# Optimization experiments

Measured on AMD Instinct MI355X. Metric: run time of the kernel, lower is better.

The kernel has to match this reference:

```python
import jax, jax.numpy as jnp
import numpy as np

N_EMBD = 384
N_HEAD = 6
HEAD_DIM = N_EMBD // N_HEAD


def setup_inputs() -> dict:
    key = jax.random.key(0)
    k1, k2, k3, k4, k5 = jax.random.split(key, 5)
    B, T, C = 256, 165, N_EMBD
    x = jax.random.normal(k1, (B, T, C), dtype=jnp.float32)
    # nn.Linear stores weight as [out, in]; we keep [in, out] for x @ W
    s = 1.0 / np.sqrt(C)
    w_qkv = jax.random.uniform(k2, (C, 3 * C), minval=-s, maxval=s, dtype=jnp.float32)
    b_qkv = jax.random.uniform(k3, (3 * C,), minval=-s, maxval=s, dtype=jnp.float32)
    w_proj = jax.random.uniform(k4, (C, C), minval=-s, maxval=s, dtype=jnp.float32)
    b_proj = jax.random.uniform(k5, (C,), minval=-s, maxval=s, dtype=jnp.float32)
    return {"x": x, "w_qkv": w_qkv, "b_qkv": b_qkv, "w_proj": w_proj, "b_proj": b_proj}


def _attn(x, w_qkv, b_qkv, w_proj, b_proj):
    B, T, C = x.shape
    qkv = x @ w_qkv + b_qkv                      # [B, T, 3C]
    q, k, v = jnp.split(qkv, 3, axis=-1)
    def heads(t):
        return t.reshape(B, T, N_HEAD, HEAD_DIM).transpose(0, 2, 1, 3)  # [B,H,T,D]
    q, k, v = heads(q), heads(k), heads(v)
    scale = 1.0 / np.sqrt(HEAD_DIM)
    scores = jnp.einsum("bhqd,bhkd->bhqk", q, k) * scale  # [B,H,T,T]
    # mask: all True except last row attends only to the last column
    row = jnp.arange(T)[:, None]
    col = jnp.arange(T)[None, :]
    allowed = (row != T - 1) | (col == T - 1)              # [T,T] bool
    scores = jnp.where(allowed, scores, -jnp.inf)
    attn = jax.nn.softmax(scores, axis=-1)
    y = jnp.einsum("bhqk,bhkd->bhqd", attn, v)             # [B,H,T,D]
    y = y.transpose(0, 2, 1, 3).reshape(B, T, C)
    return y @ w_proj + b_proj


def reference(x, w_qkv, b_qkv, w_proj, b_proj):
    return _attn(x, w_qkv, b_qkv, w_proj, b_proj)
```

## Files before the change

### kernel.cpp

```cpp
#include <hip/hip_runtime.h>


typedef __attribute__((ext_vector_type(8))) short s16x8;
typedef __attribute__((ext_vector_type(4))) float f32x4;

__device__ __forceinline__ ushort f2b(float f) {
  union { float f; unsigned u; } v; v.f = f;
  unsigned u = v.u;
  return (ushort)((u + 0x7FFFu + ((u >> 16) & 1u)) >> 16);
}

__device__ __forceinline__ void gload_lds16(const ushort* g, ushort* l) {
  __builtin_amdgcn_global_load_lds((const __attribute__((address_space(1))) void*)g,
                                   (__attribute__((address_space(3))) void*)l, 16, 0, 0);
}

__global__ __launch_bounds__(256) void prep(const float* __restrict__ x,
                                            const float* __restrict__ wq,
                                            const float* __restrict__ wp,
                                            ushort* __restrict__ xb,
                                            ushort* __restrict__ wqT,
                                            ushort* __restrict__ wpT)
{
  const int stride = gridDim.x * 256;
  const int i0 = blockIdx.x * 256 + threadIdx.x;
  for (int i = i0; i < 4055040; i += stride) {
    float4 v = ((const float4*)x)[i];
    ushort4 h = make_ushort4(f2b(v.x), f2b(v.y), f2b(v.z), f2b(v.w));
    ((ushort4*)xb)[i] = h;
  }
  for (int i = i0; i < 110592; i += stride) {
    const int n = i / 96, k4 = (i % 96) * 4;
    ushort4 h = make_ushort4(f2b(wq[(size_t)(k4 + 0) * 1152 + n]),
                             f2b(wq[(size_t)(k4 + 1) * 1152 + n]),
                             f2b(wq[(size_t)(k4 + 2) * 1152 + n]),
                             f2b(wq[(size_t)(k4 + 3) * 1152 + n]));
    *(ushort4*)(wqT + (size_t)n * 384 + k4) = h;
  }
  for (int i = i0; i < 36864; i += stride) {
    const int n = i / 96, k4 = (i % 96) * 4;
    ushort4 h = make_ushort4(f2b(wp[(size_t)(k4 + 0) * 384 + n]),
                             f2b(wp[(size_t)(k4 + 1) * 384 + n]),
                             f2b(wp[(size_t)(k4 + 2) * 384 + n]),
                             f2b(wp[(size_t)(k4 + 3) * 384 + n]));
    *(ushort4*)(wpT + (size_t)n * 384 + k4) = h;
  }
}

template<int NB, int NOUT, bool OUT_F32>
__global__ __launch_bounds__(256) void gemm_bias(const ushort* __restrict__ A,
                                                 const ushort* __restrict__ Bt,
                                                 const float* __restrict__ bias,
                                                 void* __restrict__ Out)
{
  __shared__ __align__(16) ushort Asm[2][128][64];
  __shared__ __align__(16) ushort Bsm[2][128][64];
  const int tid  = threadIdx.x;
  const int lane = tid & 63;
  const int wave = tid >> 6;
  const int wr = wave >> 1, wc = wave & 1;

  const int nwg = gridDim.x;
  const int qch = nwg >> 3, rch = nwg & 7;
  const int xcd = blockIdx.x & 7, idx = blockIdx.x >> 3;
  const int nl = (xcd < rch) ? xcd * (qch + 1) + idx
                             : rch * (qch + 1) + (xcd - rch) * qch + idx;
  const int n0 = (nl % NB) * 128;
  const int m0 = (nl / NB) * 128;

  const ushort* Ag = A  + (size_t)(m0 + (tid >> 3)) * 384 + ((tid & 7) << 3);
  const ushort* Bg = Bt + (size_t)(n0 + (tid >> 3)) * 384 + ((tid & 7) << 3);

  f32x4 acc[4][4] = {};

#define STAGE(buf, k0)                                              \
  {                                                                 \
    ushort* at_ = (ushort*)Asm[buf] + tid * 8;                      \
    ushort* bt_ = (ushort*)Bsm[buf] + tid * 8;                      \
    _Pragma("unroll")                                               \
    for (int i = 0; i < 4; ++i) {                                   \
      gload_lds16(Ag + (k0) + i * 32 * 384, at_ + i * 2048);        \
      gload_lds16(Bg + (k0) + i * 32 * 384, bt_ + i * 2048);        \
    }                                                               \
  }

  STAGE(0, 0);
  #pragma unroll
  for (int t = 0; t < 6; ++t) {
    const int cur = t & 1;
    if (t < 5) {
      STAGE(cur ^ 1, (t + 1) * 64);
      asm volatile("s_waitcnt vmcnt(8)" ::: "memory");
    } else {
      asm volatile("s_waitcnt vmcnt(0)" ::: "memory");
    }
    __builtin_amdgcn_s_barrier();
    #pragma unroll
    for (int ks = 0; ks < 2; ++ks) {
      const int kk = (ks << 5) + ((lane >> 4) << 3);
      s16x8 a[4], b[4];
      #pragma unroll
      for (int mi = 0; mi < 4; ++mi)
        a[mi] = *(const s16x8*)(&Asm[cur][(wr << 6) + (mi << 4) + (lane & 15)][kk]);
      #pragma unroll
      for (int ni = 0; ni < 4; ++ni)
        b[ni] = *(const s16x8*)(&Bsm[cur][(wc << 6) + (ni << 4) + (lane & 15)][kk]);
      #pragma unroll
      for (int mi = 0; mi < 4; ++mi) {
        #pragma unroll
        for (int ni = 0; ni < 4; ++ni)
          acc[mi][ni] = __builtin_amdgcn_mfma_f32_16x16x32_bf16(a[mi], b[ni], acc[mi][ni], 0, 0, 0);
      }
    }
    __builtin_amdgcn_s_barrier();
  }
#undef STAGE

  #pragma unroll
  for (int mi = 0; mi < 4; ++mi) {
    #pragma unroll
    for (int ni = 0; ni < 4; ++ni) {
      const int col = n0 + (wc << 6) + (ni << 4) + (lane & 15);
      const float bv = bias[col];
      #pragma unroll
      for (int r = 0; r < 4; ++r) {
        const int row = m0 + (wr << 6) + (mi << 4) + ((lane >> 4) << 2) + r;
        const float v = acc[mi][ni][r] + bv;
        if (OUT_F32) ((float*)Out)[(size_t)row * NOUT + col] = v;
        else         ((ushort*)Out)[(size_t)row * NOUT + col] = f2b(v);
      }
    }
  }
}

__global__ __launch_bounds__(256) void attn_kernel(const ushort* __restrict__ QKV,
                                                   ushort* __restrict__ Y)
{
  __shared__ __align__(16) ushort Ksm[165][64];
  __shared__ __align__(16) ushort Vtsm[64][168];
  __shared__ __align__(16) ushort Psm[4][16][168];
  const int bh = blockIdx.x;
  const int b = bh / 6, h = bh % 6;
  const int tid = threadIdx.x, lane = tid & 63, wave = tid >> 6;
  const size_t base = (size_t)b * 165 * 1152 + (size_t)h * 64;

  for (int idx = tid; idx < 165 * 8; idx += 256) {
    const int t = idx >> 3, d8 = (idx & 7) << 3;
    *(uint4*)(&Ksm[t][d8]) = *(const uint4*)(QKV + base + (size_t)t * 1152 + 384 + d8);
  }
  for (int idx = tid; idx < 165 * 8; idx += 256) {
    const int t = idx >> 3, d8 = (idx & 7) << 3;
    uint4 v = *(const uint4*)(QKV + base + (size_t)t * 1152 + 768 + d8);
    const ushort* pv = (const ushort*)&v;
    #pragma unroll
    for (int j = 0; j < 8; ++j) Vtsm[d8 + j][t] = pv[j];
  }
  for (int idx = tid; idx < 64 * 3; idx += 256) Vtsm[idx / 3][165 + idx % 3] = 0;
  __syncthreads();

  const int colv = lane & 15;
  const int grp  = lane >> 4;
  for (int it = 0; it < 3; ++it) {
    const int qt = wave + (it << 2);
    const bool active = qt < 11;
    if (active) {
      const int tq = qt * 16 + colv;
      const int tqc = tq > 164 ? 164 : tq;
      const ushort* qrow = QKV + base + (size_t)tqc * 1152;
      const s16x8 qf0 = *(const s16x8*)(qrow + (grp << 3));
      const s16x8 qf1 = *(const s16x8*)(qrow + 32 + (grp << 3));
      f32x4 s[11];
      #pragma unroll
      for (int ct = 0; ct < 11; ++ct) {
        const int col = ct * 16 + colv;
        s16x8 kb0 = {}, kb1 = {};
        if (col < 165) {
          kb0 = *(const s16x8*)(&Ksm[col][grp << 3]);
          kb1 = *(const s16x8*)(&Ksm[col][32 + (grp << 3)]);
        }
        f32x4 a = {};
        a = __builtin_amdgcn_mfma_f32_16x16x32_bf16(qf0, kb0, a, 0, 0, 0);
        a = __builtin_amdgcn_mfma_f32_16x16x32_bf16(qf1, kb1, a, 0, 0, 0);
        s[ct] = a * 0.125f;
      }
      #pragma unroll
      for (int r = 0; r < 4; ++r) {
        float m = -1e30f;
        #pragma unroll
        for (int ct = 0; ct < 11; ++ct)
          if (ct * 16 + colv < 165) m = fmaxf(m, s[ct][r]);
        #pragma unroll
        for (int off = 1; off < 16; off <<= 1) m = fmaxf(m, __shfl_xor(m, off));
        float sum = 0.f;
        #pragma unroll
        for (int ct = 0; ct < 11; ++ct) {
          const float p = (ct * 16 + colv < 165) ? __expf(s[ct][r] - m) : 0.f;
          s[ct][r] = p;
          sum += p;
        }
        #pragma unroll
        for (int off = 1; off < 16; off <<= 1) sum += __shfl_xor(sum, off);
        const float inv = 1.f / sum;
        #pragma unroll
        for (int ct = 0; ct < 11; ++ct) s[ct][r] *= inv;
      }
      #pragma unroll
      for (int ct = 0; ct < 11; ++ct) {
        const int col = ct * 16 + colv;
        if (col < 168) {
          #pragma unroll
          for (int r = 0; r < 4; ++r)
            Psm[wave][(grp << 2) + r][col] = f2b(s[ct][r]);
        }
      }
    }
    __syncthreads();
    if (active) {
      f32x4 ya[4] = {};
      #pragma unroll
      for (int ksv = 0; ksv < 6; ++ksv) {
        const int kk = (ksv << 5) + (grp << 3);
        s16x8 pa = {};
        if (kk <= 160) pa = *(const s16x8*)(&Psm[wave][colv][kk]);
        #pragma unroll
        for (int nt = 0; nt < 4; ++nt) {
          s16x8 vb = {};
          if (kk <= 160) vb = *(const s16x8*)(&Vtsm[nt * 16 + colv][kk]);
          ya[nt] = __builtin_amdgcn_mfma_f32_16x16x32_bf16(pa, vb, ya[nt], 0, 0, 0);
        }
      }
      #pragma unroll
      for (int nt = 0; nt < 4; ++nt) {
        #pragma unroll
        for (int r = 0; r < 4; ++r) {
          const int trow = qt * 16 + (grp << 2) + r;
          if (trow < 165) {
            const int d = nt * 16 + colv;
            ushort val;
            if (trow == 164) val = QKV[base + (size_t)164 * 1152 + 768 + d];
            else             val = f2b(ya[nt][r]);
            Y[((size_t)b * 165 + trow) * 384 + h * 64 + d] = val;
          }
        }
      }
    }
    __syncthreads();
  }
}

extern "C" void kernel_launch(void* const* d_in, const int* in_sizes, int n_in,
                              void* d_out, int out_size, void* d_ws, size_t ws_size,
                              hipStream_t stream) {
  const float* x      = (const float*)d_in[0];
  const float* w_qkv  = (const float*)d_in[1];
  const float* b_qkv  = (const float*)d_in[2];
  const float* w_proj = (const float*)d_in[3];
  const float* b_proj = (const float*)d_in[4];
  float* out = (float*)d_out;

  char* ws = (char*)d_ws;
  ushort* xb  = (ushort*)ws;
  ushort* wqT = (ushort*)(ws + 32440320);
  ushort* wpT = (ushort*)(ws + 33325056);
  ushort* qkv = (ushort*)(ws + 33619968);
  ushort* y   = xb;

  prep<<<1024, 256, 0, stream>>>(x, w_qkv, w_proj, xb, wqT, wpT);
  gemm_bias<9, 1152, false><<<2970, 256, 0, stream>>>(xb, wqT, b_qkv, qkv);
  attn_kernel<<<1536, 256, 0, stream>>>(qkv, y);
  gemm_bias<3, 384, true><<<990, 256, 0, stream>>>(y, wpT, b_proj, out);
}
```

Before: 261.2 us.

## Compute transposed scores in registers and feed P directly to PV MFMA

The attention kernel now computes S^T (K as the A operand) so each lane holds a full key column slice, which lets P be packed to bf16 in registers and fed straight into 16x16x16 MFMAs without the Psm shared-memory round trip or the mid-loop barriers. K is read directly from global instead of being staged in LDS, and V is staged as paired-bf16 32-bit words. Softmax uses exp2 with a folded log2e scale, rcp, and packed bf16 conversion instructions, and occupancy is hinted with launch_bounds(256,4). The risk is that uncached global K reads repeat across waves, and the smaller MFMA shape issues more instructions.

```diff
diff --git a/kernel.cpp b/kernel.cpp
--- a/kernel.cpp
+++ b/kernel.cpp
@@ -2,6 +2,7 @@
 
 
 typedef __attribute__((ext_vector_type(8))) short s16x8;
+typedef __attribute__((ext_vector_type(4))) short s16x4;
 typedef __attribute__((ext_vector_type(4))) float f32x4;
 
 __device__ __forceinline__ ushort f2b(float f) {
@@ -14,6 +15,29 @@
   __builtin_amdgcn_global_load_lds((const __attribute__((address_space(1))) void*)g,
                                    (__attribute__((address_space(3))) void*)l, 16, 0, 0);
 }
+
+#if __has_builtin(__builtin_amdgcn_mfma_f32_16x16x16bf16_1k)
+__device__ __forceinline__ f32x4 mfma16x16x16(s16x4 a, s16x4 b, f32x4 c) {
+  return __builtin_amdgcn_mfma_f32_16x16x16bf16_1k(a, b, c, 0, 0, 0);
+}
+#else
+__device__ __forceinline__ f32x4 mfma16x16x16(s16x4 a, s16x4 b, f32x4 c) {
+  asm("v_mfma_f32_16x16x16_bf16 %0, %1, %2, %0" : "+v"(c) : "v"(a), "v"(b));
+  return c;
+}
+#endif
+
+#if __has_builtin(__builtin_amdgcn_exp2f)
+#define EXP2F(x) __builtin_amdgcn_exp2f(x)
+#else
+#define EXP2F(x) __expf((x) * 0.6931471805599453f)
+#endif
+
+#if __has_builtin(__builtin_amdgcn_rcpf)
+#define RCPF(x) __builtin_amdgcn_rcpf(x)
+#else
+#define RCPF(x) (1.0f / (x))
+#endif
 
 __global__ __launch_bounds__(256) void prep(const float* __restrict__ x,
                                             const float* __restrict__ wq,
@@ -133,118 +157,125 @@
   }
 }
 
-__global__ __launch_bounds__(256) void attn_kernel(const ushort* __restrict__ QKV,
-                                                   ushort* __restrict__ Y)
+__global__ __launch_bounds__(256, 4) void attn_kernel(const ushort* __restrict__ QKV,
+                                                      ushort* __restrict__ Y)
 {
-  __shared__ __align__(16) ushort Ksm[165][64];
-  __shared__ __align__(16) ushort Vtsm[64][168];
-  __shared__ __align__(16) ushort Psm[4][16][168];
+  __shared__ uint Vt32[64][85];
   const int bh = blockIdx.x;
   const int b = bh / 6, h = bh % 6;
   const int tid = threadIdx.x, lane = tid & 63, wave = tid >> 6;
+  const int colv = lane & 15, grp = lane >> 4;
   const size_t base = (size_t)b * 165 * 1152 + (size_t)h * 64;
-
-  for (int idx = tid; idx < 165 * 8; idx += 256) {
-    const int t = idx >> 3, d8 = (idx & 7) << 3;
-    *(uint4*)(&Ksm[t][d8]) = *(const uint4*)(QKV + base + (size_t)t * 1152 + 384 + d8);
-  }
-  for (int idx = tid; idx < 165 * 8; idx += 256) {
-    const int t = idx >> 3, d8 = (idx & 7) << 3;
-    uint4 v = *(const uint4*)(QKV + base + (size_t)t * 1152 + 768 + d8);
-    const ushort* pv = (const ushort*)&v;
-    #pragma unroll
-    for (int j = 0; j < 8; ++j) Vtsm[d8 + j][t] = pv[j];
-  }
-  for (int idx = tid; idx < 64 * 3; idx += 256) Vtsm[idx / 3][165 + idx % 3] = 0;
+  const ushort* Vg = QKV + base + 768;
+
+  for (int idx = tid; idx < 85 * 8; idx += 256) {
+    const int tp = idx >> 3, d8 = (idx & 7) << 3;
+    const int t0 = 2 * tp, t1 = t0 + 1;
+    uint4 a  = *(const uint4*)(Vg + (size_t)(t0 > 164 ? 164 : t0) * 1152 + d8);
+    uint4 bv = *(const uint4*)(Vg + (size_t)(t1 > 164 ? 164 : t1) * 1152 + d8);
+    if (t0 > 164) a  = make_uint4(0, 0, 0, 0);
+    if (t1 > 164) bv = make_uint4(0, 0, 0, 0);
+    const ushort* au = (const ushort*)&a;
+    const ushort* bu = (const ushort*)&bv;
+    #pragma unroll
+    for (int j = 0; j < 8; ++j)
+      Vt32[d8 + j][tp] = (uint)au[j] | ((uint)bu[j] << 16);
+  }
   __syncthreads();
 
-  const int colv = lane & 15;
-  const int grp  = lane >> 4;
   for (int it = 0; it < 3; ++it) {
     const int qt = wave + (it << 2);
-    const bool active = qt < 11;
-    if (active) {
-      const int tq = qt * 16 + colv;
-      const int tqc = tq > 164 ? 164 : tq;
-      const ushort* qrow = QKV + base + (size_t)tqc * 1152;
-      const s16x8 qf0 = *(const s16x8*)(qrow + (grp << 3));
-      const s16x8 qf1 = *(const s16x8*)(qrow + 32 + (grp << 3));
-      f32x4 s[11];
-      #pragma unroll
-      for (int ct = 0; ct < 11; ++ct) {
-        const int col = ct * 16 + colv;
-        s16x8 kb0 = {}, kb1 = {};
-        if (col < 165) {
-          kb0 = *(const s16x8*)(&Ksm[col][grp << 3]);
-          kb1 = *(const s16x8*)(&Ksm[col][32 + (grp << 3)]);
+    if (qt >= 11) continue;
+    const int qrow = qt * 16 + colv;
+    const ushort* qp = QKV + base + (size_t)(qrow > 164 ? 164 : qrow) * 1152;
+    const s16x8 qf0 = *(const s16x8*)(qp + (grp << 3));
+    const s16x8 qf1 = *(const s16x8*)(qp + 32 + (grp << 3));
+
+    f32x4 s[11];
+    #pragma unroll
+    for (int ct = 0; ct < 11; ++ct) {
+      const int kr = ct * 16 + colv;
+      const ushort* kp = QKV + base + (size_t)(kr > 164 ? 164 : kr) * 1152 + 384;
+      const s16x8 kf0 = *(const s16x8*)(kp + (grp << 3));
+      const s16x8 kf1 = *(const s16x8*)(kp + 32 + (grp << 3));
+      f32x4 a = {};
+      a = __builtin_amdgcn_mfma_f32_16x16x32_bf16(kf0, qf0, a, 0, 0, 0);
+      a = __builtin_amdgcn_mfma_f32_16x16x32_bf16(kf1, qf1, a, 0, 0, 0);
+      s[ct] = a * 0.18033688011112042f;
+    }
+    #pragma unroll
+    for (int r = 0; r < 4; ++r)
+      if (4 * grp + r >= 5) s[10][r] = -1e30f;
+
+    float m = -1e30f;
+    #pragma unroll
+    for (int ct = 0; ct < 11; ++ct)
+      m = fmaxf(m, fmaxf(fmaxf(s[ct][0], s[ct][1]), fmaxf(s[ct][2], s[ct][3])));
+    m = fmaxf(m, __shfl_xor(m, 16));
+    m = fmaxf(m, __shfl_xor(m, 32));
+    float sm0 = 0.f, sm1 = 0.f, sm2 = 0.f, sm3 = 0.f;
+    #pragma unroll
+    for (int ct = 0; ct < 11; ++ct) {
+      const float p0 = EXP2F(s[ct][0] - m), p1 = EXP2F(s[ct][1] - m);
+      const float p2 = EXP2F(s[ct][2] - m), p3 = EXP2F(s[ct][3] - m);
+      s[ct][0] = p0; s[ct][1] = p1; s[ct][2] = p2; s[ct][3] = p3;
+      sm0 += p0; sm1 += p1; sm2 += p2; sm3 += p3;
+    }
+    float sum = (sm0 + sm1) + (sm2 + sm3);
+    sum += __shfl_xor(sum, 16);
+    sum += __shfl_xor(sum, 32);
+    const float inv = RCPF(sum);
+
+    s16x4 pk[11];
+    #pragma unroll
+    for (int ct = 0; ct < 11; ++ct) {
+      uint w0, w1;
+      float p0 = s[ct][0] * inv, p1 = s[ct][1] * inv;
+      float p2 = s[ct][2] * inv, p3 = s[ct][3] * inv;
+      asm("v_cvt_pk_bf16_f32 %0, %1, %2" : "=v"(w0) : "v"(p0), "v"(p1));
+      asm("v_cvt_pk_bf16_f32 %0, %1, %2" : "=v"(w1) : "v"(p2), "v"(p3));
+      uint* pw = (uint*)&pk[ct];
+      pw[0] = w0; pw[1] = w1;
+    }
+
+    f32x4 ya[4] = {};
+    #pragma unroll
+    for (int ct = 0; ct < 11; ++ct) {
+      const int kk2 = 8 * ct + 2 * grp;
+      #pragma unroll
+      for (int dt = 0; dt < 4; ++dt) {
+        uint w0 = 0, w1 = 0;
+        if (!(ct == 10 && grp >= 2)) {
+          w0 = Vt32[dt * 16 + colv][kk2];
+          w1 = Vt32[dt * 16 + colv][kk2 + 1];
         }
-        f32x4 a = {};
-        a = __builtin_amdgcn_mfma_f32_16x16x32_bf16(qf0, kb0, a, 0, 0, 0);
-        a = __builtin_amdgcn_mfma_f32_16x16x32_bf16(qf1, kb1, a, 0, 0, 0);
-        s[ct] = a * 0.125f;
+        s16x4 vb;
+        uint* vw = (uint*)&vb;
+        vw[0] = w0; vw[1] = w1;
+        ya[dt] = mfma16x16x16(vb, pk[ct], ya[dt]);
       }
-      #pragma unroll
-      for (int r = 0; r < 4; ++r) {
-        float m = -1e30f;
+    }
+
+    const int trow = qt * 16 + colv;
+    if (trow <= 164) {
+      ushort* yrow = Y + ((size_t)b * 165 + trow) * 384 + h * 64;
+      if (trow == 164) {
         #pragma unroll
-        for (int ct = 0; ct < 11; ++ct)
-          if (ct * 16 + colv < 165) m = fmaxf(m, s[ct][r]);
+        for (int dt = 0; dt < 4; ++dt) {
+          const int d0 = dt * 16 + (grp << 2);
+          *(uint2*)(yrow + d0) = *(const uint2*)(Vg + (size_t)164 * 1152 + d0);
+        }
+      } else {
         #pragma unroll
-        for (int off = 1; off < 16; off <<= 1) m = fmaxf(m, __shfl_xor(m, off));
-        float sum = 0.f;
-        #pragma unroll
-        for (int ct = 0; ct < 11; ++ct) {
-          const float p = (ct * 16 + colv < 165) ? __expf(s[ct][r] - m) : 0.f;
-          s[ct][r] = p;
-          sum += p;
-        }
-        #pragma unroll
-        for (int off = 1; off < 16; off <<= 1) sum += __shfl_xor(sum, off);
-        const float inv = 1.f / sum;
-        #pragma unroll
-        for (int ct = 0; ct < 11; ++ct) s[ct][r] *= inv;
-      }
-      #pragma unroll
-      for (int ct = 0; ct < 11; ++ct) {
-        const int col = ct * 16 + colv;
-        if (col < 168) {
-          #pragma unroll
-          for (int r = 0; r < 4; ++r)
-            Psm[wave][(grp << 2) + r][col] = f2b(s[ct][r]);
+        for (int dt = 0; dt < 4; ++dt) {
+          uint w0, w1;
+          asm("v_cvt_pk_bf16_f32 %0, %1, %2" : "=v"(w0) : "v"(ya[dt][0]), "v"(ya[dt][1]));
+          asm("v_cvt_pk_bf16_f32 %0, %1, %2" : "=v"(w1) : "v"(ya[dt][2]), "v"(ya[dt][3]));
+          const int d0 = dt * 16 + (grp << 2);
+          *(uint2*)(yrow + d0) = make_uint2(w0, w1);
         }
       }
     }
-    __syncthreads();
-    if (active) {
-      f32x4 ya[4] = {};
-      #pragma unroll
-      for (int ksv = 0; ksv < 6; ++ksv) {
-        const int kk = (ksv << 5) + (grp << 3);
-        s16x8 pa = {};
-        if (kk <= 160) pa = *(const s16x8*)(&Psm[wave][colv][kk]);
-        #pragma unroll
-        for (int nt = 0; nt < 4; ++nt) {
-          s16x8 vb = {};
-          if (kk <= 160) vb = *(const s16x8*)(&Vtsm[nt * 16 + colv][kk]);
-          ya[nt] = __builtin_amdgcn_mfma_f32_16x16x32_bf16(pa, vb, ya[nt], 0, 0, 0);
-        }
-      }
-      #pragma unroll
-      for (int nt = 0; nt < 4; ++nt) {
-        #pragma unroll
-        for (int r = 0; r < 4; ++r) {
-          const int trow = qt * 16 + (grp << 2) + r;
-          if (trow < 165) {
-            const int d = nt * 16 + colv;
-            ushort val;
-            if (trow == 164) val = QKV[base + (size_t)164 * 1152 + 768 + d];
-            else             val = f2b(ya[nt][r]);
-            Y[((size_t)b * 165 + trow) * 384 + h * 64 + d] = val;
-          }
-        }
-      }
-    }
-    __syncthreads();
   }
 }
 
```

New measurement: 270.4 us. 1.04x slower.
